# Kernel optimization log

Hardware: AMD Instinct MI355X
Metric: run time of the kernel (lower is better)

## Reference

```python
import jax, jax.numpy as jnp
import numpy as np
import math

B, T, C, H, S = 2, 2048, 1024, 16, 16
HD = C // H
EPS = 1e-5


def setup_inputs() -> dict:
    key = jax.random.key(0)
    ks = jax.random.split(key, 20)
    sc = 1.0 / math.sqrt(C)
    inp = {
        "x": jax.random.normal(ks[0], (B, T, C), jnp.float32),
        # A_log_fwd: log(arange(1..S)) repeated over dim (as in __init__)
        "A_log": jnp.log(jnp.tile(jnp.arange(1, S + 1, dtype=jnp.float32), (C, 1))),
        # Linear weights stored (in, out); apply as x @ W + b
        "Wd": jax.random.normal(ks[1], (C, C), jnp.float32) * sc,
        "bd": jnp.full((C,), -3.0, jnp.float32),
        "WB": jax.random.normal(ks[2], (C, S), jnp.float32) * sc,
        "WC": jax.random.normal(ks[3], (C, S), jnp.float32) * sc,
        "Wq": jax.random.normal(ks[4], (C, C), jnp.float32) * sc,
        "bq": jnp.zeros((C,), jnp.float32),
        "Wk": jax.random.normal(ks[5], (C, C), jnp.float32) * sc,
        "bk": jnp.zeros((C,), jnp.float32),
        "Wv": jax.random.normal(ks[6], (C, C), jnp.float32) * sc,
        "bv": jnp.zeros((C,), jnp.float32),
        "Wx": jax.random.normal(ks[7], (C, C), jnp.float32) * sc,
        "bx": jnp.zeros((C,), jnp.float32),
        "Wo": jax.random.normal(ks[8], (C, C), jnp.float32) * sc,
        "bo": jnp.zeros((C,), jnp.float32),
        "ln_g": jnp.ones((C,), jnp.float32),
        "ln_b": jnp.zeros((C,), jnp.float32),
        "temp": jnp.full((1, H, 1, 1), 0.5, jnp.float32),
    }
    return inp


def _forward(x, A_log, Wd, bd, WB, WC, Wq, bq, Wk, bk, Wv, bv, Wx, bx, Wo, bo, ln_g, ln_b, temp):
    x_base = x @ Wx + bx                      # (B,T,C)
    delta = jax.nn.softplus(x @ Wd + bd)      # (B,T,C)
    B_mat = x @ WB                            # (B,T,S)
    C_mat = x @ WC                            # (B,T,S)
    A = -jnp.exp(A_log)                       # (C,S)

    def scan_fn(h, inp):
        xb_t, d_t, B_t, C_t = inp             # (B,C),(B,C),(B,S),(B,S)
        bar_A = jnp.exp(d_t[..., None] * A)   # (B,C,S)
        h = bar_A * h + (d_t * xb_t)[..., None] * B_t[:, None, :]
        y = jnp.einsum('bcs,bs->bc', h, C_t)
        return h, y

    h0 = jnp.zeros((B, C, S), x.dtype)
    xs = (jnp.swapaxes(x_base, 0, 1), jnp.swapaxes(delta, 0, 1),
          jnp.swapaxes(B_mat, 0, 1), jnp.swapaxes(C_mat, 0, 1))
    _, ys = jax.lax.scan(scan_fn, h0, xs)
    out_fwd = jnp.swapaxes(ys, 0, 1)          # (B,T,C)

    # LayerNorm(x_base + out_fwd)
    hyb = x_base + out_fwd
    mu = hyb.mean(-1, keepdims=True)
    var = hyb.var(-1, keepdims=True)
    hybrid = (hyb - mu) * jax.lax.rsqrt(var + EPS) * ln_g + ln_b

    def heads(W, b):
        return (hybrid @ W + b).reshape(B, T, H, HD).transpose(0, 2, 1, 3)

    Q, K, V = heads(Wq, bq), heads(Wk, bk), heads(Wv, bv)
    scores = jnp.einsum('bhqd,bhkd->bhqk', Q, K) / math.sqrt(HD)
    scores = scores * jax.nn.softplus(temp)
    mask = jnp.tril(jnp.ones((T, T), bool))
    scores = jnp.where(mask[None, None], scores, -jnp.inf)
    attn = jax.nn.softmax(scores, axis=-1)
    out = jnp.einsum('bhqk,bhkd->bhqd', attn, V).transpose(0, 2, 1, 3).reshape(B, T, C)
    return out @ Wo + bo


def reference(x, A_log, Wd, bd, WB, WC, Wq, bq, Wk, bk, Wv, bv, Wx, bx, Wo, bo, ln_g, ln_b, temp):
    return _forward(x, A_log, Wd, bd, WB, WC, Wq, bq, Wk, bk, Wv, bv, Wx, bx, Wo, bo, ln_g, ln_b, temp)
```

## Files before the change

### kernel.cpp

```cpp
#include <hip/hip_runtime.h>
#include <math.h>

#define B_  2
#define T_  2048
#define C_  1024
#define H_  16
#define S_  16
#define HD_ 64
#define NCH 32
#define CHL 64

typedef short  short8  __attribute__((ext_vector_type(8)));
typedef unsigned short ushort8 __attribute__((ext_vector_type(8)));
typedef unsigned short ushort4v __attribute__((ext_vector_type(4)));
typedef float  f32x4   __attribute__((ext_vector_type(4)));

__device__ __forceinline__ float softplus_f(float v) {
    return fmaxf(v, 0.f) + log1pf(__expf(-fabsf(v)));
}

__device__ __forceinline__ unsigned short f2bf(float x) {
    unsigned u = __float_as_uint(x);
    u += 0x7fffu + ((u >> 16) & 1u);
    return (unsigned short)(u >> 16);
}

__device__ __forceinline__ float bf2f(unsigned short u) {
    return __uint_as_float(((unsigned)u) << 16);
}

__device__ __forceinline__ void gload16(const unsigned short* g,
                                        unsigned short* l)
{
    __builtin_amdgcn_global_load_lds(
        (const __attribute__((address_space(1))) unsigned int*)g,
        (__attribute__((address_space(3))) unsigned int*)l, 16, 0, 0);
}

__global__ __launch_bounds__(256) void cast_bf16(const float* __restrict__ in,
                                                 unsigned short* __restrict__ out,
                                                 int n4)
{
    int i = blockIdx.x * 256 + threadIdx.x;
    if (i >= n4) return;
    float4 v = ((const float4*)in)[i];
    ushort4v o = {f2bf(v.x), f2bf(v.y), f2bf(v.z), f2bf(v.w)};
    ((ushort4v*)out)[i] = o;
}

__device__ __forceinline__ void wtrans_body(const float* __restrict__ W,
                                            unsigned short* __restrict__ WT,
                                            int bx, int by, int tid)
{
    __shared__ float t[32][33];
    const int n0 = bx * 32, k0 = by * 32;
    const int tx = tid & 31, ty = tid >> 5;
#pragma unroll
    for (int p = 0; p < 4; ++p)
        t[ty + p * 8][tx] = W[(size_t)(k0 + ty + p * 8) * C_ + n0 + tx];
    __syncthreads();
#pragma unroll
    for (int p = 0; p < 4; ++p)
        WT[(size_t)(n0 + ty + p * 8) * C_ + k0 + tx] = f2bf(t[tx][ty + p * 8]);
}

__global__ __launch_bounds__(256) void wtrans(const float* __restrict__ W,
                                              unsigned short* __restrict__ WT)
{
    wtrans_body(W, WT, blockIdx.x, blockIdx.y, threadIdx.x);
}

__global__ __launch_bounds__(256) void wtrans_multi(
    const float* __restrict__ Wx, const float* __restrict__ Wd,
    const float* __restrict__ Wq, const float* __restrict__ Wk,
    const float* __restrict__ Wv,
    unsigned short* __restrict__ Astack, unsigned short* __restrict__ Wqkv)
{
    const float* src;
    unsigned short* dst;
    switch (blockIdx.z) {
        case 0: src = Wx; dst = Astack; break;
        case 1: src = Wd; dst = Astack + (size_t)1024 * 1024; break;
        case 2: src = Wq; dst = Wqkv; break;
        case 3: src = Wk; dst = Wqkv + (size_t)1024 * 1024; break;
        default: src = Wv; dst = Wqkv + (size_t)2048 * 1024; break;
    }
    wtrans_body(src, dst, blockIdx.x, blockIdx.y, threadIdx.x);
}

__global__ __launch_bounds__(256) void prep_misc(
    const float* __restrict__ WB, const float* __restrict__ WC,
    const float* __restrict__ bx, const float* __restrict__ bd,
    const float* __restrict__ bq, const float* __restrict__ bk,
    const float* __restrict__ bv,
    unsigned short* __restrict__ Astack, float* __restrict__ biasPD,
    float* __restrict__ biasQKV)
{
    int gid = blockIdx.x * 256 + threadIdx.x;
    if (gid < 32768) {
        int w = gid >> 14, rem = gid & 16383;
        int s = rem >> 10, k = rem & 1023;
        const float* src = w ? WC : WB;
        Astack[(size_t)(2048 + w * 16 + s) * 1024 + k] = f2bf(src[k * 16 + s]);
    } else {
        int id = gid - 32768;
        if (id < 2176) {
            biasPD[id] = id < 1024 ? bx[id] : (id < 2048 ? bd[id - 1024] : 0.f);
        } else {
            int id2 = id - 2176;
            if (id2 < 3072)
                biasQKV[id2] = id2 < 1024 ? bq[id2]
                             : (id2 < 2048 ? bk[id2 - 1024] : bv[id2 - 2048]);
        }
    }
}

__global__ __launch_bounds__(256) void gemm_mfma(
    const unsigned short* __restrict__ A, const unsigned short* __restrict__ Bm,
    const float* __restrict__ bias,
    void* __restrict__ outv,
    int M, int N, int K, int lda)
{
    __shared__ __align__(16) unsigned short As[4][4096];
    __shared__ __align__(16) unsigned short Bs[4][4096];

    const int tid = threadIdx.x;
    const int w = tid >> 6, lane = tid & 63;
    const int lq = lane & 15, lg = lane >> 4;
    const int wm = w >> 1, wn = w & 1;
    const int mBase = blockIdx.y * 128, nBase = blockIdx.x * 128;

    const int c0 = tid, c1 = tid + 256;
    const int rA0 = ((c0 >> 6) << 4) + (c0 & 15), kO0 = ((c0 >> 4) & 3) << 3;
    const int rA1 = ((c1 >> 6) << 4) + (c1 & 15), kO1 = ((c1 >> 4) & 3) << 3;

    const int wL0 = w * 512;
    const int wL1 = 2048 + w * 512;

    f32x4 acc[4][4];
#pragma unroll
    for (int i = 0; i < 4; ++i)
#pragma unroll
        for (int j = 0; j < 4; ++j) acc[i][j] = (f32x4){0.f, 0.f, 0.f, 0.f};

    const unsigned short* ga0 = A  + (size_t)(mBase + rA0) * lda + kO0;
    const unsigned short* ga1 = A  + (size_t)(mBase + rA1) * lda + kO1;
    const unsigned short* gb0 = Bm + (size_t)(nBase + rA0) * lda + kO0;
    const unsigned short* gb1 = Bm + (size_t)(nBase + rA1) * lda + kO1;

    #define STAGE(bufv, k0v)                               \
        do {                                               \
            gload16(ga0 + (k0v), &As[bufv][wL0]);          \
            gload16(ga1 + (k0v), &As[bufv][wL1]);          \
            gload16(gb0 + (k0v), &Bs[bufv][wL0]);          \
            gload16(gb1 + (k0v), &Bs[bufv][wL1]);          \
        } while (0)
    #define COMPUTE(bufv)                                                       \
        do {                                                                    \
            short8 a[4], b[4];                                                  \
            _Pragma("unroll")                                                   \
            for (int i = 0; i < 4; ++i)                                         \
                a[i] = *(const short8*)&As[bufv][((wm * 4 + i) * 64 + lg * 16 + lq) * 8]; \
            _Pragma("unroll")                                                   \
            for (int j = 0; j < 4; ++j)                                         \
                b[j] = *(const short8*)&Bs[bufv][((wn * 4 + j) * 64 + lg * 16 + lq) * 8]; \
            _Pragma("unroll")                                                   \
            for (int i = 0; i < 4; ++i)                                         \
                _Pragma("unroll")                                               \
                for (int j = 0; j < 4; ++j)                                     \
                    acc[i][j] = __builtin_amdgcn_mfma_f32_16x16x32_bf16(        \
                        a[i], b[j], acc[i][j], 0, 0, 0);                        \
        } while (0)
    #define WAITV4() asm volatile("s_waitcnt vmcnt(4)" ::: "memory")
    #define WAITV0() asm volatile("s_waitcnt vmcnt(0)" ::: "memory")
    #define LGKM0()  asm volatile("s_waitcnt lgkmcnt(0)" ::: "memory")
    #define STEP(cbuf, kt)                                          \
        do {                                                        \
            if ((kt) + 32 < K) WAITV4(); else WAITV0();             \
            LGKM0();                                                \
            __builtin_amdgcn_s_barrier();                           \
            if ((kt) + 64 < K) STAGE(((cbuf) + 2) & 3, (kt) + 64);  \
            COMPUTE(cbuf);                                          \
        } while (0)

    STAGE(0, 0);
    STAGE(1, 32);

    for (int k0 = 0; k0 < K; k0 += 128) {
        STEP(0, k0);
        STEP(1, k0 + 32);
        STEP(2, k0 + 64);
        STEP(3, k0 + 96);
    }
    #undef STAGE
    #undef COMPUTE
    #undef WAITV4
    #undef WAITV0
    #undef LGKM0
    #undef STEP

    float* O = (float*)outv;
#pragma unroll
    for (int j = 0; j < 4; ++j) {
        int Cg = nBase + wn * 64 + j * 16 + lq;
        float bb = bias[Cg];
#pragma unroll
        for (int i = 0; i < 4; ++i) {
            int Rb = mBase + wm * 64 + i * 16 + lg * 4;
#pragma unroll
            for (int r = 0; r < 4; ++r)
                O[(size_t)(Rb + r) * N + Cg] = acc[i][j][r] + bb;
        }
    }
}

__global__ __launch_bounds__(512, 2) void gemm_projT(
    const unsigned short* __restrict__ A, const unsigned short* __restrict__ Bm,
    const float* __restrict__ bias,
    unsigned short* __restrict__ xbaseT, unsigned short* __restrict__ deltaT,
    float* __restrict__ BmT, float* __restrict__ CmT,
    int K, int lda)
{
    __shared__ __align__(16) unsigned short AS[2][2][4096];
    __shared__ __align__(16) unsigned short BS[2][2][8192];

    const int tid = threadIdx.x;
    const int w = tid >> 6, lane = tid & 63;
    const int lq = lane & 15, lg = lane >> 4;
    const int wm = w >> 2, wn = w & 3;
    const int mBase = blockIdx.y * 128, nBase = blockIdx.x * 256;

    const int rA = ((tid >> 6) << 4) | (tid & 15);
    const int kA = ((tid >> 4) & 3) << 3;
    const unsigned short* gA = A + (size_t)(mBase + rA) * lda + kA;
    const int eA = tid * 8;
    const int c0 = tid, c1 = tid + 512;
    const int rB0 = ((c0 >> 6) << 4) | (c0 & 15), kB0 = ((c0 >> 4) & 3) << 3;
    const int rB1 = ((c1 >> 6) << 4) | (c1 & 15), kB1 = ((c1 >> 4) & 3) << 3;
    const unsigned short* gB0 = Bm + (size_t)(nBase + rB0) * lda + kB0;
    const unsigned short* gB1 = Bm + (size_t)(nBase + rB1) * lda + kB1;

    f32x4 acc[4][4];
#pragma unroll
    for (int i = 0; i < 4; ++i)
#pragma unroll
        for (int j = 0; j < 4; ++j) acc[i][j] = (f32x4){0.f, 0.f, 0.f, 0.f};

    #define STG(buf_, half_, kb_)                                             \
        do {                                                                  \
            gload16(gA  + (kb_) + (half_) * 32, &AS[buf_][half_][eA]);        \
            gload16(gB0 + (kb_) + (half_) * 32, &BS[buf_][half_][c0 * 8]);    \
            gload16(gB1 + (kb_) + (half_) * 32, &BS[buf_][half_][c1 * 8]);    \
        } while (0)
    #define WAITV6() asm volatile("s_waitcnt vmcnt(6)" ::: "memory")
    #define WAITV3() asm volatile("s_waitcnt vmcnt(3)" ::: "memory")
    #define WAITV0() asm volatile("s_waitcnt vmcnt(0)" ::: "memory")

    #define PHASE(buf_, half_, STAGE_STMT, GATE_STMT)                         \
        do {                                                                  \
            short8 a_[4], b_[4];                                              \
            _Pragma("unroll")                                                 \
            for (int i = 0; i < 4; ++i)                                       \
                a_[i] = *(const short8*)&AS[buf_][half_]                      \
                    [((wm * 4 + i) * 64 + lg * 16 + lq) * 8];                 \
            _Pragma("unroll")                                                 \
            for (int j = 0; j < 4; ++j)                                       \
                b_[j] = *(const short8*)&BS[buf_][half_]                      \
                    [((wn * 4 + j) * 64 + lg * 16 + lq) * 8];                 \
            STAGE_STMT;                                                       \
            __builtin_amdgcn_s_barrier();                                     \
            asm volatile("s_waitcnt lgkmcnt(0)" ::: "memory");                \
            __builtin_amdgcn_s_setprio(1);                                    \
            _Pragma("unroll")                                                 \
            for (int i = 0; i < 4; ++i)                                       \
                _Pragma("unroll")                                             \
                for (int j = 0; j < 4; ++j)                                   \
                    acc[i][j] = __builtin_amdgcn_mfma_f32_16x16x32_bf16(      \
                        a_[i], b_[j], acc[i][j], 0, 0, 0);                    \
            __builtin_amdgcn_s_setprio(0);                                    \
            GATE_STMT;                                                        \
            __builtin_amdgcn_s_barrier();                                     \
        } while (0)

    STG(0, 0, 0);
    STG(0, 1, 0);
    STG(1, 0, 64);
    WAITV6();
    __builtin_amdgcn_s_barrier();

    const int NT = K >> 6;
    for (int kt = 0; kt < NT; ++kt) {
        const int buf = kt & 1, nbuf = buf ^ 1;
        const int kb1 = (kt + 1) << 6, kb2 = (kt + 2) << 6;
        PHASE(buf, 0, { if (kt + 1 < NT) STG(nbuf, 1, kb1); },
              { if (kt < NT - 1) WAITV6(); else WAITV3(); });
        PHASE(buf, 1, { if (kt + 2 < NT) STG(buf, 0, kb2); },
              { if (kt < NT - 2) WAITV6();
                else if (kt == NT - 2) WAITV3(); else WAITV0(); });
    }
    #undef STG
    #undef WAITV6
    #undef WAITV3
    #undef WAITV0
    #undef PHASE

#pragma unroll
    for (int i = 0; i < 4; ++i) {
        int Rb = mBase + wm * 64 + i * 16 + lg * 4;
        if (Rb >= 2080) continue;
        float bb[4];
#pragma unroll
        for (int r = 0; r < 4; ++r) bb[r] = bias[Rb + r];
#pragma unroll
        for (int j = 0; j < 4; ++j) {
            int Cg = nBase + wn * 64 + j * 16 + lq;
            int b = Cg >> 11, t = Cg & (T_ - 1);
#pragma unroll
            for (int r = 0; r < 4; ++r) {
                int R = Rb + r;
                float v = acc[i][j][r] + bb[r];
                if (Rb < 1024) {
                    xbaseT[((size_t)b * C_ + R) * T_ + t] = f2bf(v);
                } else if (Rb < 2048) {
                    deltaT[((size_t)b * C_ + (R - 1024)) * T_ + t] =
                        f2bf(softplus_f(v));
                } else if (Rb < 2064) {
                    BmT[((size_t)b * S_ + (R - 2048)) * T_ + t] = v;
                } else {
                    CmT[((size_t)b * S_ + (R - 2064)) * T_ + t] = v;
                }
            }
        }
    }
}

__global__ __launch_bounds__(512, 2) void gemm_mfma256(
    const unsigned short* __restrict__ A, const unsigned short* __restrict__ Bm,
    const float* __restrict__ bias,
    void* __restrict__ outv, void* __restrict__ out2,
    void* __restrict__ out3,
    int M, int N, int K, int lda)
{
    __shared__ __align__(16) unsigned short AS[2][2][8192];
    __shared__ __align__(16) unsigned short BS[2][2][8192];

    const int tid = threadIdx.x;
    const int w = tid >> 6, lane = tid & 63;
    const int lq = lane & 15, lg = lane >> 4;
    const int wm = w >> 2, wn = w & 3;
    const int mBase = blockIdx.y * 256, nBase = blockIdx.x * 256;

    const int c0 = tid, c1 = tid + 512;
    const int r0 = ((c0 >> 6) << 4) | (c0 & 15), k0l = ((c0 >> 4) & 3) << 3;
    const int r1 = ((c1 >> 6) << 4) | (c1 & 15), k1l = ((c1 >> 4) & 3) << 3;
    const unsigned short* gA0 = A  + (size_t)(mBase + r0) * lda + k0l;
    const unsigned short* gA1 = A  + (size_t)(mBase + r1) * lda + k1l;
    const unsigned short* gB0 = Bm + (size_t)(nBase + r0) * lda + k0l;
    const unsigned short* gB1 = Bm + (size_t)(nBase + r1) * lda + k1l;

    f32x4 acc[8][4];
#pragma unroll
    for (int i = 0; i < 8; ++i)
#pragma unroll
        for (int j = 0; j < 4; ++j) acc[i][j] = (f32x4){0.f, 0.f, 0.f, 0.f};

    #define STG_A(buf_, half_, kb_)                                           \
        do {                                                                  \
            gload16(gA0 + (kb_) + (half_) * 32, &AS[buf_][half_][c0 * 8]);    \
            gload16(gA1 + (kb_) + (half_) * 32, &AS[buf_][half_][c1 * 8]);    \
        } while (0)
    #define STG_B(buf_, half_, kb_)                                           \
        do {                                                                  \
            gload16(gB0 + (kb_) + (half_) * 32, &BS[buf_][half_][c0 * 8]);    \
            gload16(gB1 + (kb_) + (half_) * 32, &BS[buf_][half_][c1 * 8]);    \
        } while (0)
    #define WAITV8() asm volatile("s_waitcnt vmcnt(8)" ::: "memory")
    #define WAITV4() asm volatile("s_waitcnt vmcnt(4)" ::: "memory")
    #define WAITV0() asm volatile("s_waitcnt vmcnt(0)" ::: "memory")

    #define PHASE(buf_, half_, qi_, STAGE_STMT, GATE_STMT)                    \
        do {                                                                  \
            short8 a_[4];                                                     \
            _Pragma("unroll")                                                 \
            for (int i = 0; i < 4; ++i)                                       \
                a_[i] = *(const short8*)&AS[buf_][half_]                      \
                    [((wm * 8 + (qi_) * 4 + i) * 64 + lg * 16 + lq) * 8];     \
            if ((qi_) == 0) {                                                 \
                _Pragma("unroll")                                             \
                for (int j = 0; j < 4; ++j)                                   \
                    bfr[j] = *(const short8*)&BS[buf_][half_]                 \
                        [((wn * 4 + j) * 64 + lg * 16 + lq) * 8];             \
            }                                                                 \
            STAGE_STMT;                                                       \
            __builtin_amdgcn_s_barrier();                                     \
            asm volatile("s_waitcnt lgkmcnt(0)" ::: "memory");                \
            __builtin_amdgcn_s_setprio(1);                                    \
            _Pragma("unroll")                                                 \
            for (int i = 0; i < 4; ++i)                                       \
                _Pragma("unroll")                                             \
                for (int j = 0; j < 4; ++j)                                   \
                    acc[(qi_) * 4 + i][j] =                                   \
                        __builtin_amdgcn_mfma_f32_16x16x32_bf16(              \
                            a_[i], bfr[j], acc[(qi_) * 4 + i][j], 0, 0, 0);   \
            __builtin_amdgcn_s_setprio(0);                                    \
            GATE_STMT;                                                        \
            __builtin_amdgcn_s_barrier();                                     \
        } while (0)

    STG_A(0, 0, 0);
    STG_B(0, 0, 0);
    STG_A(0, 1, 0);
    STG_B(0, 1, 0);
    STG_A(1, 0, 64);
    STG_B(1, 0, 64);
    WAITV8();
    __builtin_amdgcn_s_barrier();

    const int NT = K >> 6;
    for (int kt = 0; kt < NT; ++kt) {
        const int buf = kt & 1, nbuf = buf ^ 1;
        const int kb1 = (kt + 1) << 6, kb2 = (kt + 2) << 6;
        short8 bfr[4];
        PHASE(buf, 0, 0, { if (kt + 1 < NT) STG_A(nbuf, 1, kb1); }, {});
        PHASE(buf, 0, 1, { if (kt + 1 < NT) STG_B(nbuf, 1, kb1); },
              { if (kt < NT - 1) WAITV8(); else WAITV0(); });
        PHASE(buf, 1, 0, { if (kt + 2 < NT) STG_A(buf, 0, kb2); }, {});
        PHASE(buf, 1, 1, { if (kt + 2 < NT) STG_B(buf, 0, kb2); },
              { if (kt < NT - 2) WAITV8();
                else if (kt == NT - 2) WAITV4(); });
    }
    #undef STG_A
    #undef STG_B
    #undef WAITV8
    #undef WAITV4
    #undef WAITV0
    #undef PHASE

    unsigned short* Qb  = (unsigned short*)outv;
    unsigned short* Kb  = (unsigned short*)out2;
    unsigned short* VTb = (unsigned short*)out3;
#pragma unroll
    for (int j = 0; j < 4; ++j) {
        int Cg = nBase + wn * 64 + j * 16 + lq;
        int reg = Cg >> 10, c = Cg & 1023;
        int h = c >> 6, hd = c & 63;
        float bb = bias[Cg];
#pragma unroll
        for (int i = 0; i < 8; ++i) {
            int Rb = mBase + wm * 128 + i * 16 + lg * 4;
#pragma unroll
            for (int r = 0; r < 4; ++r) {
                int R = Rb + r, b = R >> 11, t = R & (T_ - 1);
                unsigned short o = f2bf(acc[i][j][r] + bb);
                if (reg == 0)
                    Qb[(((size_t)(b * H_ + h) * T_ + t) * HD_) + hd] = o;
                else if (reg == 1)
                    Kb[(((size_t)(b * H_ + h) * T_ + t) * HD_) + hd] = o;
                else
                    VTb[(((size_t)(b * H_ + h) * HD_ + hd) * T_) + t] = o;
            }
        }
    }
}

__global__ __launch_bounds__(256) void scan_partial(
    const unsigned short* __restrict__ xbaseT,
    const unsigned short* __restrict__ deltaT,
    const float* __restrict__ BmT, const float* __restrict__ A_log,
    float4* __restrict__ Pbuf, float4* __restrict__ Lbuf)
{
    __shared__ float bs[CHL * 16];
    const int tid = threadIdx.x;
    const int cg = blockIdx.x & 3;
    const int k  = (blockIdx.x >> 2) & (NCH - 1);
    const int b  = blockIdx.x >> 7;
    const int c  = cg * 256 + tid;
    const int tb = k * CHL;

    {
        int t0 = tid & 63, sg = (tid >> 6) << 2;
#pragma unroll
        for (int j = 0; j < 4; ++j)
            bs[t0 * 16 + sg + j] =
                BmT[((size_t)(b * S_ + sg + j)) * T_ + tb + t0];
    }
    float a[16];
#pragma unroll
    for (int sq = 0; sq < 4; ++sq) {
        float4 a4 = *(const float4*)&A_log[(size_t)c * S_ + sq * 4];
        a[sq * 4 + 0] = -__expf(a4.x);
        a[sq * 4 + 1] = -__expf(a4.y);
        a[sq * 4 + 2] = -__expf(a4.z);
        a[sq * 4 + 3] = -__expf(a4.w);
    }
    __syncthreads();

    const unsigned short* dp = deltaT + ((size_t)b * C_ + c) * T_ + tb;
    const unsigned short* xp = xbaseT + ((size_t)b * C_ + c) * T_ + tb;

    float h[16];
#pragma unroll
    for (int s = 0; s < 16; ++s) h[s] = 0.f;
    float sumd = 0.f;

    ushort4v d4 = *(const ushort4v*)&dp[0];
    ushort4v x4 = *(const ushort4v*)&xp[0];
    for (int t0 = 0; t0 < CHL; t0 += 4) {
        const int tn = (t0 + 4 < CHL) ? t0 + 4 : t0;
        ushort4v d4n = *(const ushort4v*)&dp[tn];
        ushort4v x4n = *(const ushort4v*)&xp[tn];
        float dv[4] = {bf2f(d4[0]), bf2f(d4[1]), bf2f(d4[2]), bf2f(d4[3])};
        float xv[4] = {bf2f(x4[0]), bf2f(x4[1]), bf2f(x4[2]), bf2f(x4[3])};
#pragma unroll
        for (int q = 0; q < 4; ++q) {
            float u = dv[q] * xv[q];
            sumd += dv[q];
            float bv[16];
#pragma unroll
            for (int sq = 0; sq < 4; ++sq) {
                float4 b4 = *(const float4*)&bs[(t0 + q) * 16 + sq * 4];
                bv[sq * 4 + 0] = b4.x; bv[sq * 4 + 1] = b4.y;
                bv[sq * 4 + 2] = b4.z; bv[sq * 4 + 3] = b4.w;
            }
#pragma unroll
            for (int s = 0; s < 16; ++s)
                h[s] = fmaf(__expf(dv[q] * a[s]), h[s], u * bv[s]);
        }
        d4 = d4n; x4 = x4n;
    }

    const size_t base = ((size_t)((b * NCH + k) << 10) + c) * 4;
#pragma unroll
    for (int sq = 0; sq < 4; ++sq) {
        float4 P4 = {__expf(a[sq * 4 + 0] * sumd), __expf(a[sq * 4 + 1] * sumd),
                     __expf(a[sq * 4 + 2] * sumd), __expf(a[sq * 4 + 3] * sumd)};
        float4 L4 = {h[sq * 4 + 0], h[sq * 4 + 1],
                     h[sq * 4 + 2], h[sq * 4 + 3]};
        Pbuf[base + sq] = P4;
        Lbuf[base + sq] = L4;
    }
}

__global__ __launch_bounds__(256) void scan_final(
    const unsigned short* __restrict__ xbaseT,
    const unsigned short* __restrict__ deltaT,
    const float* __restrict__ BmT, const float* __restrict__ CmT,
    const float* __restrict__ A_log, const float4* __restrict__ Pbuf,
    const float4* __restrict__ Lbuf, float* __restrict__ hyb)
{
    __shared__ float bs[CHL * 16];
    __shared__ float cs[CHL * 16];
    const int tid = threadIdx.x;
    const int cg = blockIdx.x & 3;
    const int k  = (blockIdx.x >> 2) & (NCH - 1);
    const int b  = blockIdx.x >> 7;
    const int c  = cg * 256 + tid;
    const int tb = k * CHL;

    {
        int t0 = tid & 63, sg = (tid >> 6) << 2;
#pragma unroll
        for (int j = 0; j < 4; ++j) {
            bs[t0 * 16 + sg + j] =
                BmT[((size_t)(b * S_ + sg + j)) * T_ + tb + t0];
            cs[t0 * 16 + sg + j] =
                CmT[((size_t)(b * S_ + sg + j)) * T_ + tb + t0];
        }
    }
    float a[16];
#pragma unroll
    for (int sq = 0; sq < 4; ++sq) {
        float4 a4 = *(const float4*)&A_log[(size_t)c * S_ + sq * 4];
        a[sq * 4 + 0] = -__expf(a4.x);
        a[sq * 4 + 1] = -__expf(a4.y);
        a[sq * 4 + 2] = -__expf(a4.z);
        a[sq * 4 + 3] = -__expf(a4.w);
    }

    float h[16];
#pragma unroll
    for (int s = 0; s < 16; ++s) h[s] = 0.f;
    for (int k2 = 0; k2 < k; ++k2) {
        const size_t b2 = ((size_t)((b * NCH + k2) << 10) + c) * 4;
#pragma unroll
        for (int sq = 0; sq < 4; ++sq) {
            float4 P4 = Pbuf[b2 + sq];
            float4 L4 = Lbuf[b2 + sq];
            h[sq * 4 + 0] = fmaf(P4.x, h[sq * 4 + 0], L4.x);
            h[sq * 4 + 1] = fmaf(P4.y, h[sq * 4 + 1], L4.y);
            h[sq * 4 + 2] = fmaf(P4.z, h[sq * 4 + 2], L4.z);
            h[sq * 4 + 3] = fmaf(P4.w, h[sq * 4 + 3], L4.w);
        }
    }
    __syncthreads();

    const unsigned short* dp = deltaT + ((size_t)b * C_ + c) * T_ + tb;
    const unsigned short* xp = xbaseT + ((size_t)b * C_ + c) * T_ + tb;
    float* hp = hyb + ((size_t)b * T_ + tb) * C_ + c;

    ushort4v d4 = *(const ushort4v*)&dp[0];
    ushort4v x4 = *(const ushort4v*)&xp[0];
    for (int t0 = 0; t0 < CHL; t0 += 4) {
        const int tn = (t0 + 4 < CHL) ? t0 + 4 : t0;
        ushort4v d4n = *(const ushort4v*)&dp[tn];
        ushort4v x4n = *(const ushort4v*)&xp[tn];
        float dv[4] = {bf2f(d4[0]), bf2f(d4[1]), bf2f(d4[2]), bf2f(d4[3])};
        float xv[4] = {bf2f(x4[0]), bf2f(x4[1]), bf2f(x4[2]), bf2f(x4[3])};
#pragma unroll
        for (int q = 0; q < 4; ++q) {
            float u = dv[q] * xv[q];
            float bv[16], cv[16];
#pragma unroll
            for (int sq = 0; sq < 4; ++sq) {
                float4 b4 = *(const float4*)&bs[(t0 + q) * 16 + sq * 4];
                float4 c4 = *(const float4*)&cs[(t0 + q) * 16 + sq * 4];
                bv[sq * 4 + 0] = b4.x; bv[sq * 4 + 1] = b4.y;
                bv[sq * 4 + 2] = b4.z; bv[sq * 4 + 3] = b4.w;
                cv[sq * 4 + 0] = c4.x; cv[sq * 4 + 1] = c4.y;
                cv[sq * 4 + 2] = c4.z; cv[sq * 4 + 3] = c4.w;
            }
#pragma unroll
            for (int s = 0; s < 16; ++s)
                h[s] = fmaf(__expf(dv[q] * a[s]), h[s], u * bv[s]);
            float y0 = 0.f, y1 = 0.f, y2 = 0.f, y3 = 0.f;
#pragma unroll
            for (int sq = 0; sq < 4; ++sq) {
                y0 = fmaf(h[sq * 4 + 0], cv[sq * 4 + 0], y0);
                y1 = fmaf(h[sq * 4 + 1], cv[sq * 4 + 1], y1);
                y2 = fmaf(h[sq * 4 + 2], cv[sq * 4 + 2], y2);
                y3 = fmaf(h[sq * 4 + 3], cv[sq * 4 + 3], y3);
            }
            hp[(size_t)(t0 + q) * C_] = xv[q] + ((y0 + y1) + (y2 + y3));
        }
        d4 = d4n; x4 = x4n;
    }
}

__global__ __launch_bounds__(256) void layernorm_kernel(
    const float* __restrict__ in, const float* __restrict__ g,
    const float* __restrict__ beta, unsigned short* __restrict__ out)
{
    const int row = blockIdx.x;
    const float* rp = in + (size_t)row * C_;
    const int c = threadIdx.x * 4;
    float4 v = *(const float4*)&rp[c];
    float sum = v.x + v.y + v.z + v.w;
    float sq = v.x * v.x + v.y * v.y + v.z * v.z + v.w * v.w;
#pragma unroll
    for (int off = 1; off < 64; off <<= 1) {
        sum += __shfl_xor(sum, off, 64);
        sq += __shfl_xor(sq, off, 64);
    }
    __shared__ float sS[4], sQ[4];
    int wave = threadIdx.x >> 6, lane = threadIdx.x & 63;
    if (lane == 0) { sS[wave] = sum; sQ[wave] = sq; }
    __syncthreads();
    sum = sS[0] + sS[1] + sS[2] + sS[3];
    sq = sQ[0] + sQ[1] + sQ[2] + sQ[3];
    const float mu = sum * (1.f / C_);
    const float var = sq * (1.f / C_) - mu * mu;
    const float rstd = rsqrtf(var + 1e-5f);
    float4 gg = *(const float4*)&g[c];
    float4 bb = *(const float4*)&beta[c];
    ushort4v o;
    o.x = f2bf((v.x - mu) * rstd * gg.x + bb.x);
    o.y = f2bf((v.y - mu) * rstd * gg.y + bb.y);
    o.z = f2bf((v.z - mu) * rstd * gg.z + bb.z);
    o.w = f2bf((v.w - mu) * rstd * gg.w + bb.w);
    *(ushort4v*)&out[(size_t)row * C_ + c] = o;
}

#define BKT 128
#define KP  72
#define VP  136
__global__ __launch_bounds__(256) void attn_mfma(
    const unsigned short* __restrict__ Q, const unsigned short* __restrict__ K,
    const unsigned short* __restrict__ VT, const float* __restrict__ temp,
    unsigned short* __restrict__ out)
{
    __shared__ __align__(16) unsigned short Ks[BKT * KP];
    __shared__ __align__(16) unsigned short Vs[80 * VP];
    __shared__ __align__(16) unsigned short Ps[64 * VP];

    const int tid = threadIdx.x;
    const int w = tid >> 6, lane = tid & 63;
    const int lq = lane & 15, lg = lane >> 4;
    const int p  = blockIdx.x & 15;
    const int bh = blockIdx.x >> 4;
    const int b = bh >> 4, h = bh & 15;

    const float scale = softplus_f(temp[h]) * 0.125f;
    const unsigned short* Qp = Q + (size_t)bh * T_ * HD_;
    const unsigned short* Kp = K + (size_t)bh * T_ * HD_;
    const unsigned short* Vp = VT + (size_t)bh * HD_ * T_;

    {
        int r = 64 + (tid >> 4), o = (tid & 15) * 8;
        ushort8 ones = {0x3f80, 0x3f80, 0x3f80, 0x3f80,
                        0x3f80, 0x3f80, 0x3f80, 0x3f80};
        *(ushort8*)&Vs[r * VP + o] = ones;
    }

    ushort8 kreg[4], vreg[4];
    #define LOADKV(jtv)                                                        \
        do {                                                                   \
            int kb = (jtv) * BKT;                                              \
            _Pragma("unroll")                                                  \
            for (int q2 = 0; q2 < 4; ++q2) {                                   \
                int c = tid + q2 * 256;                                        \
                kreg[q2] = *(const ushort8*)&Kp[(size_t)(kb + (c >> 3)) * HD_  \
                                                + (c & 7) * 8];                \
                vreg[q2] = *(const ushort8*)&Vp[(size_t)(c >> 4) * T_ + kb     \
                                                + (c & 15) * 8];               \
            }                                                                  \
        } while (0)

    for (int half = 0; half < 2; ++half) {
        const int qi = half ? p : (31 - p);
        const int qbase = qi * 64;
        const int nT = (qbase + 64 + BKT - 1) / BKT;

        short8 qf[2];
#pragma unroll
        for (int s = 0; s < 2; ++s)
            qf[s] = *(const short8*)&Qp[(size_t)(qbase + w * 16 + lq) * HD_
                                        + s * 32 + lg * 8];
        LOADKV(0);

        float m_i[4];
        f32x4 o[5];
#pragma unroll
        for (int r = 0; r < 4; ++r) m_i[r] = -INFINITY;
#pragma unroll
        for (int j = 0; j < 5; ++j) o[j] = (f32x4){0.f, 0.f, 0.f, 0.f};

        for (int jt = 0; jt < nT; ++jt) {
            const int kbase = jt * BKT;
            const bool last = (jt == nT - 1);
            __syncthreads();
#pragma unroll
            for (int q2 = 0; q2 < 4; ++q2) {
                int c = tid + q2 * 256;
                *(ushort8*)&Ks[(c >> 3) * KP + (c & 7) * 8] = kreg[q2];
                *(ushort8*)&Vs[(c >> 4) * VP + (c & 15) * 8] = vreg[q2];
            }
            __syncthreads();
            if (jt + 1 < nT) LOADKV(jt + 1);

            f32x4 sacc[8];
#pragma unroll
            for (int j = 0; j < 8; ++j) sacc[j] = (f32x4){0.f, 0.f, 0.f, 0.f};
#pragma unroll
            for (int s = 0; s < 2; ++s) {
#pragma unroll
                for (int j = 0; j < 8; ++j) {
                    short8 kf = *(const short8*)&Ks[(j * 16 + lq) * KP
                                                    + s * 32 + lg * 8];
                    sacc[j] = __builtin_amdgcn_mfma_f32_16x16x32_bf16(
                        qf[s], kf, sacc[j], 0, 0, 0);
                }
            }

#pragma unroll
            for (int r = 0; r < 4; ++r) {
                int qrow = qbase + w * 16 + lg * 4 + r;
                float sv[8];
#pragma unroll
                for (int j = 0; j < 8; ++j) {
                    sv[j] = sacc[j][r] * scale;
                    if (last && (kbase + j * 16 + lq > qrow)) sv[j] = -INFINITY;
                }
                float mx = sv[0];
#pragma unroll
                for (int j = 1; j < 8; ++j) mx = fmaxf(mx, sv[j]);
                mx = fmaxf(mx, __shfl_xor(mx, 1, 64));
                mx = fmaxf(mx, __shfl_xor(mx, 2, 64));
                mx = fmaxf(mx, __shfl_xor(mx, 4, 64));
                mx = fmaxf(mx, __shfl_xor(mx, 8, 64));
                float mnew = fmaxf(m_i[r], mx);
                float alpha = __expf(m_i[r] - mnew);
                m_i[r] = mnew;
#pragma unroll
                for (int j = 0; j < 5; ++j) o[j][r] *= alpha;
                const int prow = w * 16 + lg * 4 + r;
                const int psw = (((lg * 4 + r) >> 3) & 1) << 4;
#pragma unroll
                for (int j = 0; j < 8; ++j)
                    Ps[prow * VP + ((j * 16 + lq) ^ psw)] =
                        f2bf(__expf(sv[j] - mnew));
            }

#pragma unroll
            for (int s2 = 0; s2 < 4; ++s2) {
                const int rsw = ((lq >> 3) & 1) << 4;
                short8 pf = *(const short8*)&Ps[(w * 16 + lq) * VP
                                                + ((s2 * 32 + lg * 8) ^ rsw)];
#pragma unroll
                for (int j = 0; j < 5; ++j) {
                    short8 vf = *(const short8*)&Vs[(j * 16 + lq) * VP
                                                    + s2 * 32 + lg * 8];
                    o[j] = __builtin_amdgcn_mfma_f32_16x16x32_bf16(
                        pf, vf, o[j], 0, 0, 0);
                }
            }
        }

#pragma unroll
        for (int r = 0; r < 4; ++r) {
            float inv = 1.f / o[4][r];
            int qrow = qbase + w * 16 + lg * 4 + r;
#pragma unroll
            for (int j = 0; j < 4; ++j)
                out[((size_t)(b * T_ + qrow)) * C_ + h * 64 + j * 16 + lq] =
                    f2bf(o[j][r] * inv);
        }
    }
    #undef LOADKV
}

extern "C" void kernel_launch(void* const* d_in, const int* in_sizes, int n_in,
                              void* d_out, int out_size, void* d_ws, size_t ws_size,
                              hipStream_t stream)
{
    const float* x     = (const float*)d_in[0];
    const float* A_log = (const float*)d_in[1];
    const float* Wd    = (const float*)d_in[2];
    const float* bd    = (const float*)d_in[3];
    const float* WB    = (const float*)d_in[4];
    const float* WC    = (const float*)d_in[5];
    const float* Wq    = (const float*)d_in[6];
    const float* bq    = (const float*)d_in[7];
    const float* Wk    = (const float*)d_in[8];
    const float* bk    = (const float*)d_in[9];
    const float* Wv    = (const float*)d_in[10];
    const float* bv    = (const float*)d_in[11];
    const float* Wx    = (const float*)d_in[12];
    const float* bx    = (const float*)d_in[13];
    const float* Wo    = (const float*)d_in[14];
    const float* bo    = (const float*)d_in[15];
    const float* ln_g  = (const float*)d_in[16];
    const float* ln_b  = (const float*)d_in[17];
    const float* temp  = (const float*)d_in[18];

    char* wsb = (char*)d_ws;
    const size_t MB = 1024 * 1024;
    const size_t HMB = 512 * 1024;
    unsigned short* xb      = (unsigned short*)(wsb);
    float4* Pbuf            = (float4*)(wsb);
    float4* Lbuf            = (float4*)(wsb + 4 * MB);
    unsigned short* hybrid  = (unsigned short*)(wsb);
    unsigned short* Astack  = (unsigned short*)(wsb + 8 * MB);
    float* biasPD           = (float*)(wsb + 8 * MB + (size_t)2176 * 2048);
    float* biasQKV          = biasPD + 2176;
    unsigned short* WqkvT   = (unsigned short*)(wsb + 12 * MB + HMB);
    unsigned short* WoT     = (unsigned short*)(wsb + 18 * MB + HMB);
    unsigned short* deltaT  = (unsigned short*)(wsb + 18 * MB + HMB);
    unsigned short* xbaseT  = (unsigned short*)(wsb + 34 * MB + HMB);
    float* hyb              = (float*)(wsb + 50 * MB + HMB);
    float* BmT              = (float*)(wsb + 66 * MB + HMB);
    float* CmT              = BmT + (size_t)B_ * S_ * T_;
    unsigned short* Qb      = (unsigned short*)(wsb + 20 * MB + HMB);
    unsigned short* Kb      = (unsigned short*)(wsb + 28 * MB + HMB);
    unsigned short* VTb     = (unsigned short*)(wsb + 36 * MB + HMB);
    unsigned short* attnO   = (unsigned short*)(wsb + 44 * MB + HMB);

    cast_bf16<<<4096, 256, 0, stream>>>(x, xb, (B_ * T_ * C_) / 4);
    wtrans_multi<<<dim3(32, 32, 5), 256, 0, stream>>>(Wx, Wd, Wq, Wk, Wv,
                                                      Astack, WqkvT);
    prep_misc<<<149, 256, 0, stream>>>(WB, WC, bx, bd, bq, bk, bv,
                                       Astack, biasPD, biasQKV);

    gemm_projT<<<dim3(16, 17, 1), 512, 0, stream>>>(
        Astack, xb, biasPD, xbaseT, deltaT, BmT, CmT,
        1024, 1024);

    const int scanBlocks = B_ * NCH * 4;
    scan_partial<<<scanBlocks, 256, 0, stream>>>(xbaseT, deltaT, BmT, A_log,
                                                 Pbuf, Lbuf);
    scan_final<<<scanBlocks, 256, 0, stream>>>(xbaseT, deltaT, BmT, CmT, A_log,
                                               Pbuf, Lbuf, hyb);

    layernorm_kernel<<<B_ * T_, 256, 0, stream>>>(hyb, ln_g, ln_b, hybrid);

    gemm_mfma256<<<dim3(12, 16, 1), 512, 0, stream>>>(
        hybrid, WqkvT, biasQKV, Qb, Kb, VTb,
        4096, 3072, 1024, 1024);

    attn_mfma<<<B_ * H_ * 16, 256, 0, stream>>>(Qb, Kb, VTb, temp, attnO);

    wtrans<<<dim3(32, 32), 256, 0, stream>>>(Wo, WoT);
    gemm_mfma<<<dim3(8, 32, 1), 256, 0, stream>>>(
        attnO, WoT, bo, d_out,
        4096, 1024, 1024, 1024);
}
```

Baseline: 407.4 us.

## Restructure projT GEMM main loop into a 3-stage ring with one barrier per K-step

Replaces the two-buffer, two-half pipeline (two barriers per 64-wide K tile) in gemm_projT with a triple-buffered ring over 32-wide K slices, issuing the load two steps ahead and using a single barrier per step. The aim is fewer barriers and simpler wait accounting around the MFMA loop. In exchange, LDS use drops slightly (3 slices instead of 4), each step does less MFMA work per barrier, and the LDS reads are no longer overlapped with the global-load issue the way the old phase scheme was.

```diff
diff --git a/kernel.cpp b/kernel.cpp
--- a/kernel.cpp
+++ b/kernel.cpp
@@ -221,8 +221,8 @@
     float* __restrict__ BmT, float* __restrict__ CmT,
     int K, int lda)
 {
-    __shared__ __align__(16) unsigned short AS[2][2][4096];
-    __shared__ __align__(16) unsigned short BS[2][2][8192];
+    __shared__ __align__(16) unsigned short AS[3][4096];
+    __shared__ __align__(16) unsigned short BS[3][8192];
 
     const int tid = threadIdx.x;
     const int w = tid >> 6, lane = tid & 63;
@@ -246,63 +246,56 @@
 #pragma unroll
         for (int j = 0; j < 4; ++j) acc[i][j] = (f32x4){0.f, 0.f, 0.f, 0.f};
 
-    #define STG(buf_, half_, kb_)                                             \
-        do {                                                                  \
-            gload16(gA  + (kb_) + (half_) * 32, &AS[buf_][half_][eA]);        \
-            gload16(gB0 + (kb_) + (half_) * 32, &BS[buf_][half_][c0 * 8]);    \
-            gload16(gB1 + (kb_) + (half_) * 32, &BS[buf_][half_][c1 * 8]);    \
+    #define STG(buf_, kb_)                                         \
+        do {                                                       \
+            gload16(gA  + (kb_), &AS[0][(buf_) * 4096 + eA]);      \
+            gload16(gB0 + (kb_), &BS[0][(buf_) * 8192 + c0 * 8]);  \
+            gload16(gB1 + (kb_), &BS[0][(buf_) * 8192 + c1 * 8]);  \
         } while (0)
-    #define WAITV6() asm volatile("s_waitcnt vmcnt(6)" ::: "memory")
     #define WAITV3() asm volatile("s_waitcnt vmcnt(3)" ::: "memory")
     #define WAITV0() asm volatile("s_waitcnt vmcnt(0)" ::: "memory")
-
-    #define PHASE(buf_, half_, STAGE_STMT, GATE_STMT)                         \
-        do {                                                                  \
-            short8 a_[4], b_[4];                                              \
-            _Pragma("unroll")                                                 \
-            for (int i = 0; i < 4; ++i)                                       \
-                a_[i] = *(const short8*)&AS[buf_][half_]                      \
-                    [((wm * 4 + i) * 64 + lg * 16 + lq) * 8];                 \
-            _Pragma("unroll")                                                 \
-            for (int j = 0; j < 4; ++j)                                       \
-                b_[j] = *(const short8*)&BS[buf_][half_]                      \
-                    [((wn * 4 + j) * 64 + lg * 16 + lq) * 8];                 \
-            STAGE_STMT;                                                       \
-            __builtin_amdgcn_s_barrier();                                     \
-            asm volatile("s_waitcnt lgkmcnt(0)" ::: "memory");                \
-            __builtin_amdgcn_s_setprio(1);                                    \
-            _Pragma("unroll")                                                 \
-            for (int i = 0; i < 4; ++i)                                       \
-                _Pragma("unroll")                                             \
-                for (int j = 0; j < 4; ++j)                                   \
-                    acc[i][j] = __builtin_amdgcn_mfma_f32_16x16x32_bf16(      \
-                        a_[i], b_[j], acc[i][j], 0, 0, 0);                    \
-            __builtin_amdgcn_s_setprio(0);                                    \
-            GATE_STMT;                                                        \
-            __builtin_amdgcn_s_barrier();                                     \
-        } while (0)
-
-    STG(0, 0, 0);
-    STG(0, 1, 0);
-    STG(1, 0, 64);
-    WAITV6();
-    __builtin_amdgcn_s_barrier();
-
-    const int NT = K >> 6;
-    for (int kt = 0; kt < NT; ++kt) {
-        const int buf = kt & 1, nbuf = buf ^ 1;
-        const int kb1 = (kt + 1) << 6, kb2 = (kt + 2) << 6;
-        PHASE(buf, 0, { if (kt + 1 < NT) STG(nbuf, 1, kb1); },
-              { if (kt < NT - 1) WAITV6(); else WAITV3(); });
-        PHASE(buf, 1, { if (kt + 2 < NT) STG(buf, 0, kb2); },
-              { if (kt < NT - 2) WAITV6();
-                else if (kt == NT - 2) WAITV3(); else WAITV0(); });
+    #define LGKM0()  asm volatile("s_waitcnt lgkmcnt(0)" ::: "memory")
+
+    STG(0, 0);
+    STG(1, 32);
+
+    const int NT = K >> 5;
+    int buf = 0;
+    for (int t = 0; t < NT; ++t) {
+        if (t + 1 < NT) WAITV3(); else WAITV0();
+        LGKM0();
+        __builtin_amdgcn_s_barrier();
+        if (t + 2 < NT) {
+            int sb = buf + 2; if (sb >= 3) sb -= 3;
+            STG(sb, (t + 2) << 5);
+        }
+        {
+            const unsigned short* ab = &AS[0][buf * 4096];
+            const unsigned short* bb = &BS[0][buf * 8192];
+            short8 a_[4], b_[4];
+#pragma unroll
+            for (int i = 0; i < 4; ++i)
+                a_[i] = *(const short8*)&ab[((wm * 4 + i) * 64
+                                            + lg * 16 + lq) * 8];
+#pragma unroll
+            for (int j = 0; j < 4; ++j)
+                b_[j] = *(const short8*)&bb[((wn * 4 + j) * 64
+                                            + lg * 16 + lq) * 8];
+            __builtin_amdgcn_s_setprio(1);
+#pragma unroll
+            for (int i = 0; i < 4; ++i)
+#pragma unroll
+                for (int j = 0; j < 4; ++j)
+                    acc[i][j] = __builtin_amdgcn_mfma_f32_16x16x32_bf16(
+                        a_[i], b_[j], acc[i][j], 0, 0, 0);
+            __builtin_amdgcn_s_setprio(0);
+        }
+        buf = (buf == 2) ? 0 : buf + 1;
     }
     #undef STG
-    #undef WAITV6
     #undef WAITV3
     #undef WAITV0
-    #undef PHASE
+    #undef LGKM0
 
 #pragma unroll
     for (int i = 0; i < 4; ++i) {
```

New measurement: 516.0 us. 26.7% more time.
